# Kernel optimization log

Hardware: AMD Instinct MI355X
Metric: run time of the kernel (lower is better)

Reference implementation:

```python
import jax, jax.numpy as jnp
import numpy as np

TOP_P = 0.02
EPSILON = 0.1        # mask_epsilon
NORMALIZE_DEC = True

B, C, H, W = 8, 64, 64, 64
HC = 2048            # num_channels * hidden_channel_scale


def setup_inputs() -> dict:
    key = jax.random.key(0)
    k1, k2, k3 = jax.random.split(key, 3)
    x = jax.random.normal(k1, (B, C, H, W), dtype=jnp.float32)
    # xavier_uniform for conv weight [HC, C, 1, 1]: fan_in=C, fan_out=HC
    a = float(np.sqrt(6.0 / (C + HC)))
    W_enc = jax.random.uniform(k2, (HC, C), minval=-a, maxval=a, dtype=jnp.float32)
    b_enc = jnp.zeros((HC,), jnp.float32)
    b_dec = jnp.zeros((C,), jnp.float32)
    # pre-sampled standard Gumbel(0,1) noise (torch samples it in forward)
    gumbel = jax.random.gumbel(k3, (B, HC, H, W), dtype=jnp.float32)
    return {"x": x, "W_enc": W_enc, "b_enc": b_enc, "b_dec": b_dec, "gumbel": gumbel}


def reference(x, W_enc, b_enc, b_dec, gumbel):
    b = x.shape[0]
    # encode: center then 1x1 conv == channel GEMM
    xc = x - b_dec[None, :, None, None]
    pre = jnp.einsum('bchw,oc->bohw', xc, W_enc) + b_enc[None, :, None, None]
    n = pre.size // b                       # per-sample numel (static)
    k = max(1, int(TOP_P * n))
    flat_pre = pre.reshape(b, -1)
    std = jnp.std(flat_pre, axis=1, ddof=1)  # torch .std() is unbiased
    beta = (std * (1.0 / EPSILON + 1e-6)).reshape(b, 1, 1, 1)
    acts = jax.nn.relu(pre + beta * gumbel)
    # per-sample unstructured top-k: kthvalue(n-k+1) == (n-k)-th in sorted ascending
    aflat = acts.reshape(b, -1)
    kth = jnp.sort(aflat, axis=1)[:, n - k][:, None]
    mask = (aflat >= kth).astype(acts.dtype)
    sparse = (aflat * mask).reshape(acts.shape)
    # decoder weight: W_enc^T, L2-normalized over hidden dim (F.normalize dim=1)
    wd = W_enc.T  # [C, HC]
    if NORMALIZE_DEC:
        wd = wd / jnp.maximum(jnp.linalg.norm(wd, axis=1, keepdims=True), 1e-12)
    recon = jnp.einsum('bohw,co->bchw', sparse, wd) + b_dec[None, :, None, None]
    return recon, sparse
```

## Files before the change

kernel.cpp:

```cpp
#include <hip/hip_runtime.h>
#include <hip/hip_bf16.h>
#include <math.h>

#define NB    8
#define NC    64
#define HWP   4096
#define HCH   2048
#define NSAMP 8388608
#define KSEL  167772u
#define RECON_N 2097152
#define CAND_CAP 1048576u
#define CBUF_CAP 1536u

#define WS_CAND   0u
#define WS_WD     33554432u
#define WS_GHIST  33816576u
#define WS_MID    33882112u
#define WS_LOW    33914880u
#define WS_PART   33947648u
#define WS_NORM   34209792u
#define WS_BETA   34210048u
#define WS_BINT0  34210080u
#define WS_C1     34210112u
#define WS_REM    34210144u
#define WS_C2     34210176u
#define WS_REM2   34210208u
#define WS_KTH    34210240u
#define WS_FLAGS  34210304u
#define WS_GCNT   34210432u

__device__ __forceinline__ unsigned bf16r(float f) {
  unsigned u = __float_as_uint(f);
  unsigned r = (u >> 16) & 1u;
  return (u + 0x7fffu + r) >> 16;
}

__global__ __launch_bounds__(256) void k0a_norm(const float* __restrict__ W,
                                                float* __restrict__ normv) {
  __shared__ float red[256];
  int c = blockIdx.x, t = threadIdx.x;
  float s = 0.f;
  for (int o = t; o < HCH; o += 256) { float w = W[o * NC + c]; s += w * w; }
  red[t] = s; __syncthreads();
  for (int off = 128; off; off >>= 1) { if (t < off) red[t] += red[t + off]; __syncthreads(); }
  if (t == 0) normv[c] = fmaxf(sqrtf(red[0]), 1e-12f);
}

__global__ __launch_bounds__(256) void k0b_wd(const float* __restrict__ W,
                                              const float* __restrict__ normv,
                                              unsigned short* __restrict__ wdb) {
  int i = blockIdx.x * 256 + threadIdx.x;
  if (i < HCH * NC) wdb[i] = (unsigned short)bf16r(W[i] / normv[i & 63]);
}

__global__ __launch_bounds__(256) void k1_encode(const float* __restrict__ x,
                                                 const float* __restrict__ W,
                                                 const float* __restrict__ b_enc,
                                                 const float* __restrict__ b_dec,
                                                 float* __restrict__ pre,
                                                 double* __restrict__ part) {
  __shared__ float xs[64][128];
  __shared__ float wt[64][128];
  const int t = threadIdx.x;
  const int pt = blockIdx.x;
  const int ot = blockIdx.y;
  const int b  = blockIdx.z;
  const int p0 = pt << 7, o0 = ot << 7;

  {
    const int c  = t >> 2;
    const int pc = (t & 3) << 5;
    const float* xp = x + (((size_t)(b * NC + c)) << 12) + p0 + pc;
    const float bd = b_dec[c];
    #pragma unroll
    for (int j = 0; j < 8; j++) {
      float4 v = ((const float4*)xp)[j];
      v.x -= bd; v.y -= bd; v.z -= bd; v.w -= bd;
      *(float4*)&xs[c][pc + 4 * j] = v;
    }
    const int ol = t >> 1;
    const int c0 = (t & 1) << 5;
    const float* wp = W + (((size_t)(o0 + ol)) << 6) + c0;
    #pragma unroll
    for (int j = 0; j < 8; j++) {
      float4 w4 = ((const float4*)wp)[j];
      wt[c0 + 4 * j + 0][ol] = w4.x;
      wt[c0 + 4 * j + 1][ol] = w4.y;
      wt[c0 + 4 * j + 2][ol] = w4.z;
      wt[c0 + 4 * j + 3][ol] = w4.w;
    }
  }
  __syncthreads();

  const int og = (t >> 4) << 3;
  const int pg = (t & 15) << 3;
  float acc[8][8];
  #pragma unroll
  for (int i = 0; i < 8; i++)
    #pragma unroll
    for (int j = 0; j < 8; j++) acc[i][j] = 0.f;

  #pragma unroll 8
  for (int cc = 0; cc < 64; cc++) {
    float4 w0 = *(const float4*)&wt[cc][og];
    float4 w1 = *(const float4*)&wt[cc][og + 4];
    float4 x0 = *(const float4*)&xs[cc][pg];
    float4 x1 = *(const float4*)&xs[cc][pg + 4];
    float wv[8] = {w0.x, w0.y, w0.z, w0.w, w1.x, w1.y, w1.z, w1.w};
    float xv[8] = {x0.x, x0.y, x0.z, x0.w, x1.x, x1.y, x1.z, x1.w};
    #pragma unroll
    for (int i = 0; i < 8; i++)
      #pragma unroll
      for (int j = 0; j < 8; j++)
        acc[i][j] += wv[i] * xv[j];
  }

  double s = 0.0, s2 = 0.0;
  #pragma unroll
  for (int i = 0; i < 8; i++) {
    const float be = b_enc[o0 + og + i];
    float r[8];
    #pragma unroll
    for (int j = 0; j < 8; j++) {
      r[j] = acc[i][j] + be;
      double d = (double)r[j];
      s += d; s2 += d * d;
    }
    float* pp = pre + (((size_t)(b * HCH + o0 + og + i)) << 12) + p0 + pg;
    *(float4*)pp       = make_float4(r[0], r[1], r[2], r[3]);
    *(float4*)(pp + 4) = make_float4(r[4], r[5], r[6], r[7]);
  }
  #pragma unroll
  for (int off = 32; off; off >>= 1) { s += __shfl_down(s, off); s2 += __shfl_down(s2, off); }
  __syncthreads();
  double* redd = (double*)&xs[0][0];
  if ((t & 63) == 0) { redd[(t >> 6) * 2] = s; redd[(t >> 6) * 2 + 1] = s2; }
  __syncthreads();
  if (t == 0) {
    double ts = redd[0] + redd[2] + redd[4] + redd[6];
    double t2 = redd[1] + redd[3] + redd[5] + redd[7];
    int pidx = (b * 16 + ot) * 32 + pt;
    part[2 * pidx] = ts; part[2 * pidx + 1] = t2;
  }
}

__global__ __launch_bounds__(256) void k2_beta(const double* __restrict__ part,
                                               float* __restrict__ beta,
                                               unsigned* __restrict__ binT0) {
  __shared__ double sd[256], sd2[256];
  int b = blockIdx.x, t = threadIdx.x;
  double s = 0.0, s2 = 0.0;
  for (int j = 0; j < 2; j++) {
    int pi = b * 512 + t * 2 + j;
    s += part[2 * pi]; s2 += part[2 * pi + 1];
  }
  sd[t] = s; sd2[t] = s2; __syncthreads();
  for (int off = 128; off; off >>= 1) {
    if (t < off) { sd[t] += sd[t + off]; sd2[t] += sd2[t + off]; }
    __syncthreads();
  }
  if (t == 0) {
    const double n = (double)NSAMP;
    double var = (sd2[0] - sd[0] * sd[0] / n) / (n - 1.0);
    if (var < 0.0) var = 0.0;
    float bv = (float)(sqrt(var) * 10.000001);
    beta[b] = bv;
    binT0[b] = __float_as_uint(2.5f * bv) >> 20;
  }
}

__global__ __launch_bounds__(256) void k3_acts(float* __restrict__ acts,
                                               const float* __restrict__ gum,
                                               const float* __restrict__ beta,
                                               const unsigned* __restrict__ binT0,
                                               unsigned* __restrict__ ghist,
                                               float* __restrict__ cand,
                                               unsigned* __restrict__ gcnt,
                                               unsigned* __restrict__ flags) {
  __shared__ unsigned lh[2048];
  __shared__ float cbuf[CBUF_CAP];
  __shared__ unsigned lcnt, gbase;
  const int b = blockIdx.z;
  const float be = beta[b];
  const unsigned bT0 = binT0[b];
  const int lane = threadIdx.x & 63;
  const unsigned long long lm_lt = (1ull << lane) - 1ull;
  for (int i = threadIdx.x; i < 2048; i += 256) lh[i] = 0u;
  if (threadIdx.x == 0) lcnt = 0u;
  __syncthreads();
  float4* a4 = (float4*)(acts + ((size_t)b << 23));
  const float4* g4 = (const float4*)(gum + ((size_t)b << 23));
  const int per4 = 1 << 21;
  for (int i = blockIdx.x * 256 + threadIdx.x; i < per4; i += gridDim.x * 256) {
    float4 p = a4[i];
    float4 g = g4[i];
    float4 a;
    a.x = fmaxf(__fadd_rn(p.x, __fmul_rn(be, g.x)), 0.f);
    a.y = fmaxf(__fadd_rn(p.y, __fmul_rn(be, g.y)), 0.f);
    a.z = fmaxf(__fadd_rn(p.z, __fmul_rn(be, g.z)), 0.f);
    a.w = fmaxf(__fadd_rn(p.w, __fmul_rn(be, g.w)), 0.f);
    a4[i] = a;
    unsigned u0 = __float_as_uint(a.x), u1 = __float_as_uint(a.y);
    unsigned u2 = __float_as_uint(a.z), u3 = __float_as_uint(a.w);
    bool c0 = (a.x > 0.f) && ((u0 >> 20) >= bT0);
    bool c1 = (a.y > 0.f) && ((u1 >> 20) >= bT0);
    bool c2 = (a.z > 0.f) && ((u2 >> 20) >= bT0);
    bool c3 = (a.w > 0.f) && ((u3 >> 20) >= bT0);
    unsigned long long m0 = __ballot(c0), m1 = __ballot(c1);
    unsigned long long m2 = __ballot(c2), m3 = __ballot(c3);
    unsigned n0 = __popcll(m0), n1 = __popcll(m1), n2 = __popcll(m2), n3 = __popcll(m3);
    unsigned tot = n0 + n1 + n2 + n3;
    if (tot) {
      unsigned base = 0;
      if (lane == 0) base = atomicAdd(&lcnt, tot);
      base = (unsigned)__shfl((int)base, 0);
      unsigned i0 = base + __popcll(m0 & lm_lt);
      unsigned i1 = base + n0 + __popcll(m1 & lm_lt);
      unsigned i2 = base + n0 + n1 + __popcll(m2 & lm_lt);
      unsigned i3 = base + n0 + n1 + n2 + __popcll(m3 & lm_lt);
      if (c0 && i0 < CBUF_CAP) cbuf[i0] = a.x;
      if (c1 && i1 < CBUF_CAP) cbuf[i1] = a.y;
      if (c2 && i2 < CBUF_CAP) cbuf[i2] = a.z;
      if (c3 && i3 < CBUF_CAP) cbuf[i3] = a.w;
      if (c0) atomicAdd(&lh[u0 >> 20], 1u);
      if (c1) atomicAdd(&lh[u1 >> 20], 1u);
      if (c2) atomicAdd(&lh[u2 >> 20], 1u);
      if (c3) atomicAdd(&lh[u3 >> 20], 1u);
    }
  }
  __syncthreads();
  if (threadIdx.x == 0) {
    unsigned n = lcnt;
    if (n > CBUF_CAP) { atomicOr(&flags[b], 2u); n = CBUF_CAP; }
    unsigned gb = atomicAdd(&gcnt[b * 32], n);
    if (gb + n > CAND_CAP) atomicOr(&flags[b], 2u);
    gbase = gb;
  }
  __syncthreads();
  {
    float* candb = cand + ((size_t)b * CAND_CAP);
    const unsigned n = (lcnt > CBUF_CAP) ? CBUF_CAP : lcnt;
    const unsigned gb = gbase;
    for (unsigned i = threadIdx.x; i < n; i += 256) {
      unsigned d = gb + i;
      if (d < CAND_CAP) candb[d] = cbuf[i];
    }
  }
  for (int i = threadIdx.x; i < 2048; i += 256) {
    unsigned v = lh[i];
    if (v) atomicAdd(&ghist[(b << 11) + i], v);
  }
}

__global__ __launch_bounds__(256) void k4a_check(const unsigned* __restrict__ ghist,
                                                 unsigned* __restrict__ flags) {
  __shared__ unsigned red[256];
  int b = blockIdx.x, t = threadIdx.x;
  unsigned s = 0;
  for (int j = 0; j < 8; j++) s += ghist[(b << 11) + t * 8 + j];
  red[t] = s; __syncthreads();
  for (int off = 128; off; off >>= 1) { if (t < off) red[t] += red[t + off]; __syncthreads(); }
  if (t == 0 && red[0] < KSEL) atomicOr(&flags[b], 1u);
}

__global__ __launch_bounds__(256) void k3fb(const float* __restrict__ acts,
                                            const unsigned* __restrict__ binT0,
                                            const unsigned* __restrict__ flags,
                                            unsigned* __restrict__ ghist) {
  const int b = blockIdx.z;
  if ((flags[b] & 1u) == 0u) return;
  __shared__ unsigned lh[8192];
  const unsigned bT0 = binT0[b];
  const unsigned sub = threadIdx.x & 3;
  for (int i = threadIdx.x; i < 8192; i += 256) lh[i] = 0u;
  __syncthreads();
  const float4* a4 = (const float4*)(acts + ((size_t)b << 23));
  const int per4 = 1 << 21;
  for (int i = blockIdx.x * 256 + threadIdx.x; i < per4; i += gridDim.x * 256) {
    float4 a = a4[i];
    unsigned u;
    u = __float_as_uint(a.x);
    if (a.x > 0.f && (u >> 20) < bT0) atomicAdd(&lh[((u >> 20) << 2) | sub], 1u);
    u = __float_as_uint(a.y);
    if (a.y > 0.f && (u >> 20) < bT0) atomicAdd(&lh[((u >> 20) << 2) | sub], 1u);
    u = __float_as_uint(a.z);
    if (a.z > 0.f && (u >> 20) < bT0) atomicAdd(&lh[((u >> 20) << 2) | sub], 1u);
    u = __float_as_uint(a.w);
    if (a.w > 0.f && (u >> 20) < bT0) atomicAdd(&lh[((u >> 20) << 2) | sub], 1u);
  }
  __syncthreads();
  for (int i = threadIdx.x; i < 2048; i += 256) {
    unsigned v = lh[4 * i] + lh[4 * i + 1] + lh[4 * i + 2] + lh[4 * i + 3];
    if (v) atomicAdd(&ghist[(b << 11) + i], v);
  }
}

__global__ __launch_bounds__(256) void k4_coarse(const unsigned* __restrict__ ghist,
                                                 int* __restrict__ c1v,
                                                 int* __restrict__ remv,
                                                 float* __restrict__ kth) {
  __shared__ unsigned h[2048];
  __shared__ unsigned csum[256];
  int b = blockIdx.x, t = threadIdx.x;
  for (int i = t; i < 2048; i += 256) h[i] = ghist[(b << 11) + i];
  __syncthreads();
  unsigned cs = 0;
  for (int j = 0; j < 8; j++) cs += h[t * 8 + j];
  csum[t] = cs; __syncthreads();
  unsigned suf = 0;
  for (int tt = t + 1; tt < 256; tt++) suf += csum[tt];
  if (suf < KSEL && suf + cs >= KSEL) {
    unsigned cum = suf;
    for (int j = 7; j >= 0; j--) {
      unsigned hv = h[t * 8 + j];
      cum += hv;
      if (cum >= KSEL) { c1v[b] = t * 8 + j; remv[b] = (int)(KSEL - (cum - hv)); break; }
    }
  }
  if (t == 0) {
    unsigned tot = 0;
    for (int tt = 0; tt < 256; tt++) tot += csum[tt];
    if (tot < KSEL) { c1v[b] = -1; kth[b] = 0.f; }
  }
}

__global__ __launch_bounds__(256) void k5m(const float* __restrict__ acts,
                                           const float* __restrict__ cand,
                                           const unsigned* __restrict__ gcnt,
                                           const unsigned* __restrict__ flags,
                                           const int* __restrict__ c1v,
                                           unsigned* __restrict__ mid) {
  const int b = blockIdx.z;
  const int c1 = c1v[b];
  __shared__ unsigned lm[1024];
  for (int i = threadIdx.x; i < 1024; i += 256) lm[i] = 0u;
  __syncthreads();
  if (c1 >= 0) {
    const unsigned c1u = (unsigned)c1;
    if (flags[b] == 0u) {
      const float* candb = cand + ((size_t)b * CAND_CAP);
      const unsigned n = gcnt[b * 32];
      for (unsigned i = blockIdx.x * 256 + threadIdx.x; i < n; i += gridDim.x * 256) {
        unsigned u = __float_as_uint(candb[i]);
        if ((u >> 20) == c1u) atomicAdd(&lm[(u >> 10) & 0x3FFu], 1u);
      }
    } else {
      const float4* a4 = (const float4*)(acts + ((size_t)b << 23));
      for (int i = blockIdx.x * 256 + threadIdx.x; i < (1 << 21); i += gridDim.x * 256) {
        float4 a = a4[i];
        unsigned u;
        u = __float_as_uint(a.x);
        if (a.x > 0.f && (u >> 20) == c1u) atomicAdd(&lm[(u >> 10) & 0x3FFu], 1u);
        u = __float_as_uint(a.y);
        if (a.y > 0.f && (u >> 20) == c1u) atomicAdd(&lm[(u >> 10) & 0x3FFu], 1u);
        u = __float_as_uint(a.z);
        if (a.z > 0.f && (u >> 20) == c1u) atomicAdd(&lm[(u >> 10) & 0x3FFu], 1u);
        u = __float_as_uint(a.w);
        if (a.w > 0.f && (u >> 20) == c1u) atomicAdd(&lm[(u >> 10) & 0x3FFu], 1u);
      }
    }
  }
  __syncthreads();
  for (int i = threadIdx.x; i < 1024; i += 256) {
    unsigned v = lm[i];
    if (v) atomicAdd(&mid[(b << 10) + i], v);
  }
}

__global__ __launch_bounds__(256) void k6a(const unsigned* __restrict__ mid,
                                           const int* __restrict__ c1v,
                                           const int* __restrict__ remv,
                                           int* __restrict__ c2v,
                                           int* __restrict__ rem2v) {
  int b = blockIdx.x, t = threadIdx.x;
  if (c1v[b] < 0) return;
  __shared__ unsigned h[1024];
  __shared__ unsigned csum[256];
  for (int i = t; i < 1024; i += 256) h[i] = mid[(b << 10) + i];
  __syncthreads();
  unsigned cs = 0;
  for (int j = 0; j < 4; j++) cs += h[t * 4 + j];
  csum[t] = cs; __syncthreads();
  unsigned suf = 0;
  for (int tt = t + 1; tt < 256; tt++) suf += csum[tt];
  unsigned R = (unsigned)remv[b];
  if (suf < R && suf + cs >= R) {
    unsigned cum = suf;
    for (int j = 3; j >= 0; j--) {
      unsigned hv = h[t * 4 + j];
      cum += hv;
      if (cum >= R) { c2v[b] = t * 4 + j; rem2v[b] = (int)(R - (cum - hv)); break; }
    }
  }
}

__global__ __launch_bounds__(256) void k5l(const float* __restrict__ acts,
                                           const float* __restrict__ cand,
                                           const unsigned* __restrict__ gcnt,
                                           const unsigned* __restrict__ flags,
                                           const int* __restrict__ c1v,
                                           const int* __restrict__ c2v,
                                           unsigned* __restrict__ low) {
  const int b = blockIdx.z;
  const int c1 = c1v[b];
  __shared__ unsigned lm[1024];
  for (int i = threadIdx.x; i < 1024; i += 256) lm[i] = 0u;
  __syncthreads();
  if (c1 >= 0) {
    const unsigned key = ((unsigned)c1 << 10) | (unsigned)c2v[b];
    if (flags[b] == 0u) {
      const float* candb = cand + ((size_t)b * CAND_CAP);
      const unsigned n = gcnt[b * 32];
      for (unsigned i = blockIdx.x * 256 + threadIdx.x; i < n; i += gridDim.x * 256) {
        unsigned u = __float_as_uint(candb[i]);
        if ((u >> 10) == key) atomicAdd(&lm[u & 0x3FFu], 1u);
      }
    } else {
      const float4* a4 = (const float4*)(acts + ((size_t)b << 23));
      for (int i = blockIdx.x * 256 + threadIdx.x; i < (1 << 21); i += gridDim.x * 256) {
        float4 a = a4[i];
        unsigned u;
        u = __float_as_uint(a.x);
        if (a.x > 0.f && (u >> 10) == key) atomicAdd(&lm[u & 0x3FFu], 1u);
        u = __float_as_uint(a.y);
        if (a.y > 0.f && (u >> 10) == key) atomicAdd(&lm[u & 0x3FFu], 1u);
        u = __float_as_uint(a.z);
        if (a.z > 0.f && (u >> 10) == key) atomicAdd(&lm[u & 0x3FFu], 1u);
        u = __float_as_uint(a.w);
        if (a.w > 0.f && (u >> 10) == key) atomicAdd(&lm[u & 0x3FFu], 1u);
      }
    }
  }
  __syncthreads();
  for (int i = threadIdx.x; i < 1024; i += 256) {
    unsigned v = lm[i];
    if (v) atomicAdd(&low[(b << 10) + i], v);
  }
}

__global__ __launch_bounds__(256) void k6b(const unsigned* __restrict__ low,
                                           const int* __restrict__ c1v,
                                           const int* __restrict__ c2v,
                                           const int* __restrict__ rem2v,
                                           float* __restrict__ kth) {
  int b = blockIdx.x, t = threadIdx.x;
  int c1 = c1v[b];
  if (c1 < 0) return;
  __shared__ unsigned h[1024];
  __shared__ unsigned csum[256];
  for (int i = t; i < 1024; i += 256) h[i] = low[(b << 10) + i];
  __syncthreads();
  unsigned cs = 0;
  for (int j = 0; j < 4; j++) cs += h[t * 4 + j];
  csum[t] = cs; __syncthreads();
  unsigned suf = 0;
  for (int tt = t + 1; tt < 256; tt++) suf += csum[tt];
  unsigned R2 = (unsigned)rem2v[b];
  if (suf < R2 && suf + cs >= R2) {
    unsigned cum = suf;
    for (int j = 3; j >= 0; j--) {
      unsigned hv = h[t * 4 + j];
      cum += hv;
      if (cum >= R2) {
        unsigned bits = ((unsigned)c1 << 20) | ((unsigned)c2v[b] << 10) | (unsigned)(t * 4 + j);
        kth[b] = __uint_as_float(bits);
        break;
      }
    }
  }
}

__global__ __launch_bounds__(256, 4) void k7e_decode(float* __restrict__ acts,
                                                     const unsigned short* __restrict__ wdb,
                                                     const float* __restrict__ kthv,
                                                     float* __restrict__ pdec) {
  __shared__ unsigned xsl[64 * 64];
  __shared__ unsigned wtl[64 * 32];
  const int t = threadIdx.x;
  const int pt = blockIdx.x;
  const int kc = blockIdx.y;
  const int b  = blockIdx.z;
  const int p0 = pt << 7;
  const float kth = kthv[b];
  const int cg = t >> 5;
  const int pg = t & 31;
  const int ob0 = kc * 512;

  float acc[8][4];
  #pragma unroll
  for (int i = 0; i < 8; i++)
    #pragma unroll
    for (int j = 0; j < 4; j++) acc[i][j] = 0.f;

  for (int tile = 0; tile < 8; ++tile) {
    __syncthreads();
    #pragma unroll
    for (int k = 0; k < 8; ++k) {
      const int ol = 8 * k + (t >> 5);
      float* ap = acts + (((size_t)(b * HCH + ob0 + tile * 64 + ol)) << 12) + p0 + ((t & 31) << 2);
      float4 a0 = *(const float4*)ap;
      float4 s0;
      s0.x = (a0.x >= kth) ? a0.x : 0.f;  s0.y = (a0.y >= kth) ? a0.y : 0.f;
      s0.z = (a0.z >= kth) ? a0.z : 0.f;  s0.w = (a0.w >= kth) ? a0.w : 0.f;
      *(float4*)ap = s0;
      uint2 pk;
      pk.x = bf16r(s0.x) | (bf16r(s0.y) << 16);
      pk.y = bf16r(s0.z) | (bf16r(s0.w) << 16);
      *(uint2*)&xsl[(8 * k + (t >> 5)) * 64 + ((t & 31) << 1)] = pk;
    }
    #pragma unroll
    for (int k = 0; k < 2; ++k) {
      const int ol = 32 * k + (t >> 3);
      const uint4 w = *(const uint4*)(wdb + (((size_t)(ob0 + tile * 64 + ol)) << 6) + ((t & 7) << 3));
      *(uint4*)&wtl[1024 * k + 4 * t] = w;
    }
    __syncthreads();
    #pragma unroll 8
    for (int cc = 0; cc < 64; ++cc) {
      uint2 xv = *(const uint2*)&xsl[cc * 64 + pg * 2];
      uint4 wv = *(const uint4*)&wtl[cc * 32 + cg * 4];
      float xp[4], wf[8];
      xp[0] = __uint_as_float(xv.x << 16); xp[1] = __uint_as_float(xv.x & 0xffff0000u);
      xp[2] = __uint_as_float(xv.y << 16); xp[3] = __uint_as_float(xv.y & 0xffff0000u);
      wf[0] = __uint_as_float(wv.x << 16); wf[1] = __uint_as_float(wv.x & 0xffff0000u);
      wf[2] = __uint_as_float(wv.y << 16); wf[3] = __uint_as_float(wv.y & 0xffff0000u);
      wf[4] = __uint_as_float(wv.z << 16); wf[5] = __uint_as_float(wv.z & 0xffff0000u);
      wf[6] = __uint_as_float(wv.w << 16); wf[7] = __uint_as_float(wv.w & 0xffff0000u);
      #pragma unroll
      for (int i = 0; i < 8; i++)
        #pragma unroll
        for (int j = 0; j < 4; j++)
          acc[i][j] = fmaf(wf[i], xp[j], acc[i][j]);
    }
  }

  float* pb = pdec + (size_t)kc * RECON_N + (((size_t)(b * NC)) << 12) + p0 + pg * 4;
  #pragma unroll
  for (int i = 0; i < 8; ++i) {
    *(float4*)(pb + ((size_t)(cg * 8 + i) << 12)) =
        make_float4(acc[i][0], acc[i][1], acc[i][2], acc[i][3]);
  }
}

__global__ __launch_bounds__(256) void k8_add(const float* __restrict__ pdec,
                                              const float* __restrict__ b_dec,
                                              float* __restrict__ recon) {
  const int i = blockIdx.x * 256 + threadIdx.x;
  if (i < (RECON_N / 4)) {
    float4 a = ((const float4*)pdec)[i];
    float4 b4 = ((const float4*)pdec)[i + RECON_N / 4];
    float4 c4 = ((const float4*)pdec)[i + 2 * (RECON_N / 4)];
    float4 d4 = ((const float4*)pdec)[i + 3 * (RECON_N / 4)];
    const float bd = b_dec[(i >> 10) & 63];
    float4 r;
    r.x = ((a.x + b4.x) + c4.x) + d4.x + bd;
    r.y = ((a.y + b4.y) + c4.y) + d4.y + bd;
    r.z = ((a.z + b4.z) + c4.z) + d4.z + bd;
    r.w = ((a.w + b4.w) + c4.w) + d4.w + bd;
    ((float4*)recon)[i] = r;
  }
}

extern "C" void kernel_launch(void* const* d_in, const int* in_sizes, int n_in,
                              void* d_out, int out_size, void* d_ws, size_t ws_size,
                              hipStream_t stream) {
  const float* x     = (const float*)d_in[0];
  const float* W     = (const float*)d_in[1];
  const float* b_enc = (const float*)d_in[2];
  const float* b_dec = (const float*)d_in[3];
  const float* gum   = (const float*)d_in[4];
  float* recon  = (float*)d_out;
  float* sparse = recon + RECON_N;

  char* ws = (char*)d_ws;
  float*    cand  = (float*)(ws + WS_CAND);
  float*    pdec  = (float*)(ws + WS_CAND);
  unsigned short* wdb = (unsigned short*)(ws + WS_WD);
  unsigned* ghist = (unsigned*)(ws + WS_GHIST);
  unsigned* mid   = (unsigned*)(ws + WS_MID);
  unsigned* low   = (unsigned*)(ws + WS_LOW);
  double*   part  = (double*)(ws + WS_PART);
  float*    normv = (float*)(ws + WS_NORM);
  float*    beta  = (float*)(ws + WS_BETA);
  unsigned* binT0 = (unsigned*)(ws + WS_BINT0);
  int*      c1v   = (int*)(ws + WS_C1);
  int*      remv  = (int*)(ws + WS_REM);
  int*      c2v   = (int*)(ws + WS_C2);
  int*      rem2v = (int*)(ws + WS_REM2);
  float*    kth   = (float*)(ws + WS_KTH);
  unsigned* flags = (unsigned*)(ws + WS_FLAGS);
  unsigned* gcnt  = (unsigned*)(ws + WS_GCNT);

  hipMemsetAsync(ws + WS_GHIST, 0, 131072, stream);
  hipMemsetAsync(ws + WS_FLAGS, 0, 1152, stream);

  k0a_norm  <<<64, 256, 0, stream>>>(W, normv);
  k0b_wd    <<<512, 256, 0, stream>>>(W, normv, wdb);
  k1_encode <<<dim3(32, 16, NB), 256, 0, stream>>>(x, W, b_enc, b_dec, sparse, part);
  k2_beta   <<<NB, 256, 0, stream>>>(part, beta, binT0);
  k3_acts   <<<dim3(1024, 1, NB), 256, 0, stream>>>(sparse, gum, beta, binT0, ghist, cand, gcnt, flags);
  k4a_check <<<NB, 256, 0, stream>>>(ghist, flags);
  k3fb      <<<dim3(1024, 1, NB), 256, 0, stream>>>(sparse, binT0, flags, ghist);
  k4_coarse <<<NB, 256, 0, stream>>>(ghist, c1v, remv, kth);
  k5m       <<<dim3(256, 1, NB), 256, 0, stream>>>(sparse, cand, gcnt, flags, c1v, mid);
  k6a       <<<NB, 256, 0, stream>>>(mid, c1v, remv, c2v, rem2v);
  k5l       <<<dim3(256, 1, NB), 256, 0, stream>>>(sparse, cand, gcnt, flags, c1v, c2v, low);
  k6b       <<<NB, 256, 0, stream>>>(low, c1v, c2v, rem2v, kth);
  k7e_decode<<<dim3(32, 4, NB), 256, 0, stream>>>(sparse, wdb, kth, pdec);
  k8_add    <<<RECON_N / 4 / 256, 256, 0, stream>>>(pdec, b_dec, recon);
}
```

Baseline: 531.8 us.

## Widen decode tile to 256 pixels and split hidden dim with atomic accumulation

The decode kernel now computes an 8x8 register tile per thread over 256 pixels per block, doubling reuse of each loaded weight. The hidden dimension is split into 8 chunks of 256 instead of 4 of 512, and pairs of chunks accumulate into the four partial buffers with float atomicAdd after those buffers are zeroed by a memset. The goal is more parallelism and more FMA work per shared-memory load. In exchange it adds an extra memset, scalar atomic traffic, higher register pressure, and nondeterministic summation order.

Result: slower. 862.8 us (+62.2%).

```diff
diff --git a/kernel.cpp b/kernel.cpp
--- a/kernel.cpp
+++ b/kernel.cpp
@@ -470,43 +470,49 @@
   }
 }
 
-__global__ __launch_bounds__(256, 4) void k7e_decode(float* __restrict__ acts,
+__global__ __launch_bounds__(256, 4) void k7f_decode(float* __restrict__ acts,
                                                      const unsigned short* __restrict__ wdb,
                                                      const float* __restrict__ kthv,
                                                      float* __restrict__ pdec) {
-  __shared__ unsigned xsl[64 * 64];
+  __shared__ unsigned xsl[64 * 128];
   __shared__ unsigned wtl[64 * 32];
   const int t = threadIdx.x;
   const int pt = blockIdx.x;
   const int kc = blockIdx.y;
   const int b  = blockIdx.z;
-  const int p0 = pt << 7;
+  const int p0 = pt << 8;
   const float kth = kthv[b];
   const int cg = t >> 5;
   const int pg = t & 31;
-  const int ob0 = kc * 512;
-
-  float acc[8][4];
+  const int ob0 = kc * 256;
+
+  float acc[8][8];
   #pragma unroll
   for (int i = 0; i < 8; i++)
     #pragma unroll
-    for (int j = 0; j < 4; j++) acc[i][j] = 0.f;
-
-  for (int tile = 0; tile < 8; ++tile) {
+    for (int j = 0; j < 8; j++) acc[i][j] = 0.f;
+
+  for (int tile = 0; tile < 4; ++tile) {
     __syncthreads();
     #pragma unroll
     for (int k = 0; k < 8; ++k) {
       const int ol = 8 * k + (t >> 5);
-      float* ap = acts + (((size_t)(b * HCH + ob0 + tile * 64 + ol)) << 12) + p0 + ((t & 31) << 2);
-      float4 a0 = *(const float4*)ap;
-      float4 s0;
+      float* ap = acts + (((size_t)(b * HCH + ob0 + tile * 64 + ol)) << 12) + p0 + ((t & 31) << 3);
+      float4 a0 = ((const float4*)ap)[0];
+      float4 a1 = ((const float4*)ap)[1];
+      float4 s0, s1;
       s0.x = (a0.x >= kth) ? a0.x : 0.f;  s0.y = (a0.y >= kth) ? a0.y : 0.f;
       s0.z = (a0.z >= kth) ? a0.z : 0.f;  s0.w = (a0.w >= kth) ? a0.w : 0.f;
-      *(float4*)ap = s0;
-      uint2 pk;
+      s1.x = (a1.x >= kth) ? a1.x : 0.f;  s1.y = (a1.y >= kth) ? a1.y : 0.f;
+      s1.z = (a1.z >= kth) ? a1.z : 0.f;  s1.w = (a1.w >= kth) ? a1.w : 0.f;
+      ((float4*)ap)[0] = s0;
+      ((float4*)ap)[1] = s1;
+      uint4 pk;
       pk.x = bf16r(s0.x) | (bf16r(s0.y) << 16);
       pk.y = bf16r(s0.z) | (bf16r(s0.w) << 16);
-      *(uint2*)&xsl[(8 * k + (t >> 5)) * 64 + ((t & 31) << 1)] = pk;
+      pk.z = bf16r(s1.x) | (bf16r(s1.y) << 16);
+      pk.w = bf16r(s1.z) | (bf16r(s1.w) << 16);
+      *(uint4*)&xsl[1024 * k + 4 * t] = pk;
     }
     #pragma unroll
     for (int k = 0; k < 2; ++k) {
@@ -517,11 +523,13 @@
     __syncthreads();
     #pragma unroll 8
     for (int cc = 0; cc < 64; ++cc) {
-      uint2 xv = *(const uint2*)&xsl[cc * 64 + pg * 2];
+      uint4 xv = *(const uint4*)&xsl[cc * 128 + pg * 4];
       uint4 wv = *(const uint4*)&wtl[cc * 32 + cg * 4];
-      float xp[4], wf[8];
+      float xp[8], wf[8];
       xp[0] = __uint_as_float(xv.x << 16); xp[1] = __uint_as_float(xv.x & 0xffff0000u);
       xp[2] = __uint_as_float(xv.y << 16); xp[3] = __uint_as_float(xv.y & 0xffff0000u);
+      xp[4] = __uint_as_float(xv.z << 16); xp[5] = __uint_as_float(xv.z & 0xffff0000u);
+      xp[6] = __uint_as_float(xv.w << 16); xp[7] = __uint_as_float(xv.w & 0xffff0000u);
       wf[0] = __uint_as_float(wv.x << 16); wf[1] = __uint_as_float(wv.x & 0xffff0000u);
       wf[2] = __uint_as_float(wv.y << 16); wf[3] = __uint_as_float(wv.y & 0xffff0000u);
       wf[4] = __uint_as_float(wv.z << 16); wf[5] = __uint_as_float(wv.z & 0xffff0000u);
@@ -529,16 +537,17 @@
       #pragma unroll
       for (int i = 0; i < 8; i++)
         #pragma unroll
-        for (int j = 0; j < 4; j++)
+        for (int j = 0; j < 8; j++)
           acc[i][j] = fmaf(wf[i], xp[j], acc[i][j]);
     }
   }
 
-  float* pb = pdec + (size_t)kc * RECON_N + (((size_t)(b * NC)) << 12) + p0 + pg * 4;
+  float* pb = pdec + (size_t)(kc >> 1) * RECON_N + (((size_t)(b * NC)) << 12) + p0 + pg * 8;
   #pragma unroll
   for (int i = 0; i < 8; ++i) {
-    *(float4*)(pb + ((size_t)(cg * 8 + i) << 12)) =
-        make_float4(acc[i][0], acc[i][1], acc[i][2], acc[i][3]);
+    float* pr = pb + ((size_t)(cg * 8 + i) << 12);
+    #pragma unroll
+    for (int j = 0; j < 8; ++j) atomicAdd(pr + j, acc[i][j]);
   }
 }
 
@@ -606,6 +615,7 @@
   k6a       <<<NB, 256, 0, stream>>>(mid, c1v, remv, c2v, rem2v);
   k5l       <<<dim3(256, 1, NB), 256, 0, stream>>>(sparse, cand, gcnt, flags, c1v, c2v, low);
   k6b       <<<NB, 256, 0, stream>>>(low, c1v, c2v, rem2v, kth);
-  k7e_decode<<<dim3(32, 4, NB), 256, 0, stream>>>(sparse, wdb, kth, pdec);
+  hipMemsetAsync(ws + WS_CAND, 0, 4u * RECON_N * 4u, stream);
+  k7f_decode<<<dim3(16, 8, NB), 256, 0, stream>>>(sparse, wdb, kth, pdec);
   k8_add    <<<RECON_N / 4 / 256, 256, 0, stream>>>(pdec, b_dec, recon);
 }
```
